# Kernel optimization log

Hardware: AMD Instinct MI355X
Metric: run time of the kernel (lower is better)

Reference implementation:

```python
import jax, jax.numpy as jnp
import numpy as np

B, DIM, H, W = 16, 96, 64, 64
HID = 2 * DIM          # ffn_expansion_factor = 2
BN_EPS = 1e-5
LN_EPS = 1e-6


def _gelu(x):
    return jax.nn.gelu(x, approximate=False)  # torch F.gelu default = exact erf


def _ln(x, g, b):
    m = jnp.mean(x, axis=-1, keepdims=True)
    v = jnp.mean((x - m) ** 2, axis=-1, keepdims=True)
    return (x - m) / jnp.sqrt(v + LN_EPS) * g + b


def _dwconv2d(x, w, b):
    # x: (B,C,H,W), w: (C,1,kh,kw) depthwise
    C = x.shape[1]
    kh, kw = w.shape[2], w.shape[3]
    y = jax.lax.conv_general_dilated(
        x, w, (1, 1), [(kh // 2, kh // 2), (kw // 2, kw // 2)],
        dimension_numbers=('NCHW', 'OIHW', 'NCHW'), feature_group_count=C)
    return y + b[None, :, None, None]


def _conv_along_c(z, w, b):
    # z: (N,1,C); w: (8,1,k) -> conv over spectral/channel axis (Conv3d with (1,1,k) kernel)
    k = w.shape[2]
    y = jax.lax.conv_general_dilated(z, w, (1,), [(k // 2, k // 2)],
                                     dimension_numbers=('NCH', 'OIH', 'NCH'))
    return y + b[None, :, None]


def _bn_branch(y, g, bb):
    # eval-mode BatchNorm3d with running_mean=0, running_var=1; y: (N,8,C)
    return _gelu(y * (g / jnp.sqrt(1.0 + BN_EPS))[None, :, None] + bb[None, :, None])


def _patch_embed(z, w3a, b3a, bn3a_g, bn3a_b, w3b, b3b, bn3b_g, bn3b_b,
                 w3c, b3c, bn3c_g, bn3c_b, w2, b2, bn2_g, bn2_b):
    # z: (b,h,w,c) NHWC; PatchEmbedLayerSpa
    b_, h_, w_, c_ = z.shape
    zf = z.reshape(-1, 1, c_)
    f1 = _bn_branch(_conv_along_c(zf, w3a, b3a), bn3a_g, bn3a_b)
    f2 = _bn_branch(_conv_along_c(zf, w3b, b3b), bn3b_g, bn3b_b)
    f3 = _bn_branch(_conv_along_c(zf, w3c, b3c), bn3c_g, bn3c_b)
    cat = jnp.concatenate([f1, f2, f3], axis=1).reshape(b_, h_, w_, 24, c_)
    # 1x1 Conv2d over flattened (c y) -> dim; einsum replaces rearrange + conv
    y = jnp.einsum('bhwoy,doy->bhwd', cat, w2) + b2
    y = _gelu(y * (bn2_g / jnp.sqrt(1.0 + BN_EPS)) + bn2_b)  # eval BatchNorm2d + GELU
    return y + z


def _ffn(t, pin_w, pin_b, dw_w, dw_b, pout_w, pout_b):
    # Restormer GDFN; t: (b, c, X, Y) NCHW
    u = jnp.einsum('bcxy,oc->boxy', t, pin_w) + pin_b[None, :, None, None]
    u = _dwconv2d(u, dw_w, dw_b)
    u1, u2 = jnp.split(u, 2, axis=1)
    g = _gelu(u1) * u2
    return jnp.einsum('bcxy,oc->boxy', g, pout_w) + pout_b[None, :, None, None]


def setup_inputs() -> dict:
    key = jax.random.key(0)
    ks = iter(jax.random.split(key, 48))
    nrm = lambda shape, s=0.02: jax.random.normal(next(ks), shape, jnp.float32) * s
    d = {}
    d['x'] = jax.random.normal(next(ks), (B, DIM, H, W), jnp.float32)
    d['pos_w'] = nrm((DIM, 1, 3, 3)); d['pos_b'] = jnp.zeros((DIM,), jnp.float32)
    for n in ('ln1', 'ln2', 'ln3'):
        d[n + '_g'] = jnp.ones((DIM,), jnp.float32)
        d[n + '_b'] = jnp.zeros((DIM,), jnp.float32)
    for n, k in (('a', 3), ('b', 5), ('c', 7)):
        d['w3' + n] = nrm((8, 1, k)); d['b3' + n] = jnp.zeros((8,), jnp.float32)
        d['bn3' + n + '_g'] = jnp.ones((8,), jnp.float32)
        d['bn3' + n + '_b'] = jnp.zeros((8,), jnp.float32)
    d['w2'] = nrm((DIM, 24, DIM)); d['b2'] = jnp.zeros((DIM,), jnp.float32)
    d['bn2_g'] = jnp.ones((DIM,), jnp.float32); d['bn2_b'] = jnp.zeros((DIM,), jnp.float32)
    d['pin_w'] = nrm((2 * HID, DIM)); d['pin_b'] = jnp.zeros((2 * HID,), jnp.float32)
    d['dw_w'] = nrm((2 * HID, 1, 3, 3)); d['dw_b'] = jnp.zeros((2 * HID,), jnp.float32)
    d['pout_w'] = nrm((DIM, HID)); d['pout_b'] = jnp.zeros((DIM,), jnp.float32)
    return d


def reference(x, pos_w, pos_b, ln1_g, ln1_b, ln2_g, ln2_b, ln3_g, ln3_b,
              w3a, b3a, bn3a_g, bn3a_b, w3b, b3b, bn3b_g, bn3b_b,
              w3c, b3c, bn3c_g, bn3c_b, w2, b2, bn2_g, bn2_b,
              pin_w, pin_b, dw_w, dw_b, pout_w, pout_b):
    # pos embed dwconv + residual (NCHW)
    x = x + _dwconv2d(x, pos_w, pos_b)
    y = jnp.transpose(x, (0, 2, 3, 1))  # NHWC
    # attn4(norm3(y)) returns its input (bug in source: `out = rearrange(x, ...)`)
    y = y + _ln(y, ln3_g, ln3_b)
    # attn(norm1(y)) returns PatchEmbedLayerSpa(norm1(y)) (same bug in MGEFE)
    y = y + _patch_embed(_ln(y, ln1_g, ln1_b), w3a, b3a, bn3a_g, bn3a_b,
                         w3b, b3b, bn3b_g, bn3b_b, w3c, b3c, bn3c_g, bn3c_b,
                         w2, b2, bn2_g, bn2_b)
    y = _ln(y, ln2_g, ln2_b)
    t = jnp.transpose(y, (0, 3, 2, 1))  # (b,c,w,h) per source permute(0,3,2,1)
    f = _ffn(t, pin_w, pin_b, dw_w, dw_b, pout_w, pout_b)
    f = jnp.transpose(f, (0, 2, 3, 1))  # (b,w,h,c)
    y = f + f
    return jnp.transpose(y, (0, 3, 1, 2))  # (b,c,w,h)
```

## Files before the change

### kernel.cpp

```cpp
#include <hip/hip_runtime.h>


using bf16x8 = __attribute__((ext_vector_type(8))) short;
using f32x4  = __attribute__((ext_vector_type(4))) float;
using f32x2  = __attribute__((ext_vector_type(2))) float;

struct P {
  const float *x, *pos_w, *pos_b;
  const float *ln1g, *ln1b, *ln2g, *ln2b, *ln3g, *ln3b;
  const float *w3a, *b3a, *bn3ag, *bn3ab;
  const float *w3b, *b3b, *bn3bg, *bn3bb;
  const float *w3c, *b3c, *bn3cg, *bn3cb;
  const float *w2, *b2, *bn2g, *bn2b;
  const float *pin_w, *pin_b, *dw_w, *dw_b, *pout_w, *pout_b;
  float *y1;
  unsigned short *u;
  unsigned short *w2f;
  unsigned short *pinf;
  unsigned short *poutf;
  float *dwt;
  float *out;
};

__device__ __forceinline__ unsigned short f2bf(float f) {
  unsigned int v = __float_as_uint(f);
  v += 0x7fffu + ((v >> 16) & 1u);
  return (unsigned short)(v >> 16);
}
__device__ __forceinline__ float bf2f(unsigned short s) {
  return __uint_as_float(((unsigned int)s) << 16);
}
__device__ __forceinline__ unsigned int cvtpk(f32x2 g) {
  unsigned int pk;
  asm("v_cvt_pk_bf16_f32 %0, %1, %2" : "=v"(pk) : "v"(g.x), "v"(g.y));
  return pk;
}

__device__ __forceinline__ f32x2 gelu2p(f32x2 x) {
  f32x2 u = x * 0.70710678118654752f;
  f32x2 s = __builtin_elementwise_min(u * u, f32x2{1.f, 1.f});
  f32x2 pq = __builtin_elementwise_fma(s, f32x2{1.1283585149e-1f, 1.1283585149e-1f},
                                       f32x2{-3.7612625824e-1f, -3.7612625824e-1f});
  pq = __builtin_elementwise_fma(pq, s, f32x2{1.1283791657f, 1.1283791657f});
  f32x2 xh = x * 0.5f;
  return __builtin_elementwise_fma(xh, u * pq, xh);
}

__device__ __forceinline__ void swz_decode(int bid, int& b, int& s) {
  int xcd = bid & 7, idx = bid >> 3;
  b = xcd * 2 + (idx >> 6);
  s = idx & 63;
}

__global__ __launch_bounds__(256) void k1p(P p) {
  __shared__ float t1[96 * 65];
  if (blockIdx.x >= 1024) {
    int id = (blockIdx.x - 1024) * 256 + threadIdx.x;
    if (id < 221184) {
      int j = id & 7, l = (id >> 3) & 63, r = id >> 9;
      int ks = r % 3; r /= 3; int nt = r % 6, o = r / 6;
      int d = nt * 16 + (l & 15), y = ks * 32 + (l >> 4) * 8 + j;
      p.w2f[id] = f2bf(p.w2[(d * 24 + o) * 96 + y]);
    } else if (id < 258048) {
      int id2 = id - 221184;
      int j = id2 & 7, l = (id2 >> 3) & 63, r = id2 >> 9;
      int ks = r % 3, nt = r / 3;
      int o = nt * 16 + (l & 15), k = ks * 32 + (l >> 4) * 8 + j;
      p.pinf[id2] = f2bf(p.pin_w[o * 96 + k]);
    } else if (id < 276480) {
      int id3 = id - 258048;
      int j = id3 & 7, l = (id3 >> 3) & 63, r = id3 >> 9;
      int ks = r % 6, mt = r / 6;
      int d = mt * 16 + (l & 15), cc = ks * 32 + (l >> 4) * 8 + j;
      p.poutf[id3] = f2bf(p.pout_w[d * 192 + cc]);
    } else if (id < 279936) {
      int id4 = id - 276480;
      int tap = id4 / 384, c = id4 - tap * 384;
      p.dwt[id4] = p.dw_w[c * 9 + tap];
    }
    return;
  }

  int b, h; swz_decode(blockIdx.x, b, h);
  int bh = b * 64 + h;
  int t = threadIdx.x;
  const float* xb = p.x + (size_t)b * 96 * 4096;

  if (t < 192) {
    int c = t >> 1, w0 = (t & 1) * 32;
    const float* xc = xb + (size_t)c * 4096;
    float win[3][34];
    #pragma unroll
    for (int r = 0; r < 3; ++r) {
      int hh = h - 1 + r;
      bool v = (hh >= 0 && hh < 64);
      const float* row = xc + hh * 64;
      #pragma unroll
      for (int i = 0; i < 8; ++i) {
        float4 q = v ? *(const float4*)(row + w0 + i * 4) : make_float4(0,0,0,0);
        win[r][1+i*4] = q.x; win[r][2+i*4] = q.y;
        win[r][3+i*4] = q.z; win[r][4+i*4] = q.w;
      }
      win[r][0]  = (v && w0 > 0)  ? row[w0 - 1]  : 0.f;
      win[r][33] = (v && w0 < 32) ? row[w0 + 32] : 0.f;
    }
    float wt[9];
    #pragma unroll
    for (int i = 0; i < 9; ++i) wt[i] = p.pos_w[c * 9 + i];
    float pb = p.pos_b[c];
    #pragma unroll
    for (int w = 0; w < 32; ++w) {
      float acc = pb;
      #pragma unroll
      for (int r = 0; r < 3; ++r)
        #pragma unroll
        for (int j = 0; j < 3; ++j)
          acc = fmaf(wt[r * 3 + j], win[r][w + j], acc);
      t1[c * 65 + w0 + w] = win[1][w + 1] + acc;
    }
  }
  __syncthreads();
  {
    int w = t >> 2, c0 = (t & 3) * 24;
    float vv[24];
    float s1 = 0.f, s2 = 0.f;
    #pragma unroll
    for (int i = 0; i < 24; ++i) {
      float q = t1[(c0 + i) * 65 + w];
      vv[i] = q; s1 += q; s2 += q * q;
    }
    s1 += __shfl_xor(s1, 1); s1 += __shfl_xor(s1, 2);
    s2 += __shfl_xor(s2, 1); s2 += __shfl_xor(s2, 2);
    float m = s1 * (1.f / 96.f);
    float r = rsqrtf(fmaf(-m, m, s2 * (1.f / 96.f)) + 1e-6f);
    #pragma unroll
    for (int i = 0; i < 24; ++i) {
      int c = c0 + i;
      vv[i] += fmaf((vv[i] - m) * r, p.ln3g[c], p.ln3b[c]);
    }
    float* dst = p.y1 + (size_t)bh * 6144 + w * 96 + c0;
    #pragma unroll
    for (int i = 0; i < 6; ++i)
      *(float4*)(dst + i * 4) = make_float4(vv[i*4], vv[i*4+1], vv[i*4+2], vv[i*4+3]);
  }
}

template <int KSZ>
__device__ __forceinline__ void k2_cat(const float* __restrict__ w3, float b3v,
    float bng, float bnb, float rs, unsigned short* buf,
    const float (&zw)[30], int px, int c0) {
  float sc = bng * rs;
  float wr[KSZ];
  #pragma unroll
  for (int k = 0; k < KSZ; ++k) wr[k] = w3[k] * sc;
  float bias0 = fmaf(b3v, sc, bnb);
  constexpr int OFF = 3 - KSZ / 2;
  unsigned int packed[12];
  #pragma unroll
  for (int e2 = 0; e2 < 12; ++e2) {
    f32x2 f = {bias0, bias0};
    #pragma unroll
    for (int k = 0; k < KSZ; ++k) {
      f32x2 zp = {zw[2 * e2 + OFF + k], zw[2 * e2 + 1 + OFF + k]};
      f = __builtin_elementwise_fma(f32x2{wr[k], wr[k]}, zp, f);
    }
    packed[e2] = cvtpk(gelu2p(f));
  }
  uint4* cw = (uint4*)(buf + px * 104 + c0);
  cw[0] = *(uint4*)&packed[0];
  cw[1] = *(uint4*)&packed[4];
  cw[2] = *(uint4*)&packed[8];
}

template <int KSZ_NEXT, bool LAST>
__device__ __forceinline__ void k2_step(
    const P& p, int o, const float* __restrict__ w3n, float b3n,
    float bngn, float bnbn, float rs,
    const unsigned short* cur, unsigned short* nxt, const float (&zw)[30],
    int px, int c0, int nt0, int ar0, int ar1, f32x4 (&acc)[2][3]) {
  int lane = (threadIdx.x & 63);
  const unsigned short* wf = p.w2f + (size_t)o * 9216 + lane * 8;
  bf16x8 Ba[3], Bb[3];
  #pragma unroll
  for (int n = 0; n < 3; ++n)
    Ba[n] = *(const bf16x8*)(wf + ((nt0 + n) * 3 + 0) * 512);

  if (!LAST)
    k2_cat<KSZ_NEXT>(w3n, b3n, bngn, bnbn, rs, nxt, zw, px, c0);

  #pragma unroll
  for (int n = 0; n < 3; ++n)
    Bb[n] = *(const bf16x8*)(wf + ((nt0 + n) * 3 + 1) * 512);
  {
    bf16x8 a0 = *(const bf16x8*)&cur[ar0];
    bf16x8 a1 = *(const bf16x8*)&cur[ar1];
    #pragma unroll
    for (int n = 0; n < 3; ++n) {
      acc[0][n] = __builtin_amdgcn_mfma_f32_16x16x32_bf16(a0, Ba[n], acc[0][n], 0, 0, 0);
      acc[1][n] = __builtin_amdgcn_mfma_f32_16x16x32_bf16(a1, Ba[n], acc[1][n], 0, 0, 0);
    }
  }
  #pragma unroll
  for (int n = 0; n < 3; ++n)
    Ba[n] = *(const bf16x8*)(wf + ((nt0 + n) * 3 + 2) * 512);
  {
    bf16x8 a0 = *(const bf16x8*)&cur[ar0 + 32];
    bf16x8 a1 = *(const bf16x8*)&cur[ar1 + 32];
    #pragma unroll
    for (int n = 0; n < 3; ++n) {
      acc[0][n] = __builtin_amdgcn_mfma_f32_16x16x32_bf16(a0, Bb[n], acc[0][n], 0, 0, 0);
      acc[1][n] = __builtin_amdgcn_mfma_f32_16x16x32_bf16(a1, Bb[n], acc[1][n], 0, 0, 0);
    }
  }
  {
    bf16x8 a0 = *(const bf16x8*)&cur[ar0 + 64];
    bf16x8 a1 = *(const bf16x8*)&cur[ar1 + 64];
    #pragma unroll
    for (int n = 0; n < 3; ++n) {
      acc[0][n] = __builtin_amdgcn_mfma_f32_16x16x32_bf16(a0, Ba[n], acc[0][n], 0, 0, 0);
      acc[1][n] = __builtin_amdgcn_mfma_f32_16x16x32_bf16(a1, Ba[n], acc[1][n], 0, 0, 0);
    }
  }
  __syncthreads();
}

__global__ __launch_bounds__(256) void k2(P p) {
  __shared__ __align__(16) char smraw[26624];
  unsigned short* cat0 = (unsigned short*)smraw;
  unsigned short* cat1 = (unsigned short*)(smraw + 13312);

  int b, h; swz_decode(blockIdx.x, b, h);
  int bh = b * 64 + h;
  int t = threadIdx.x, lane = t & 63, wv = t >> 6;
  const float* yrow = p.y1 + (size_t)bh * 6144;
  int px = t >> 2, sub = t & 3, c0 = sub * 24;

  float zw[30];
  {
    float v[24];
    const float* src = yrow + px * 96 + c0;
    float s1 = 0.f, s2 = 0.f;
    #pragma unroll
    for (int i = 0; i < 6; ++i) {
      float4 q = *(const float4*)(src + i * 4);
      v[i*4] = q.x; v[i*4+1] = q.y; v[i*4+2] = q.z; v[i*4+3] = q.w;
    }
    #pragma unroll
    for (int i = 0; i < 24; ++i) { s1 += v[i]; s2 += v[i] * v[i]; }
    s1 += __shfl_xor(s1, 1); s1 += __shfl_xor(s1, 2);
    s2 += __shfl_xor(s2, 1); s2 += __shfl_xor(s2, 2);
    float m = s1 * (1.f / 96.f);
    float r = rsqrtf(fmaf(-m, m, s2 * (1.f / 96.f)) + 1e-6f);
    #pragma unroll
    for (int i = 0; i < 24; ++i) {
      int c = c0 + i;
      zw[3 + i] = fmaf((v[i] - m) * r, p.ln1g[c], p.ln1b[c]);
    }
  }
  {
    float a0 = __shfl(zw[24], lane - 1), a1 = __shfl(zw[25], lane - 1),
          a2 = __shfl(zw[26], lane - 1);
    float b0 = __shfl(zw[3], lane + 1), b1 = __shfl(zw[4], lane + 1),
          b2 = __shfl(zw[5], lane + 1);
    bool lo = (sub > 0), hi = (sub < 3);
    zw[0] = lo ? a0 : 0.f; zw[1] = lo ? a1 : 0.f; zw[2] = lo ? a2 : 0.f;
    zw[27] = hi ? b0 : 0.f; zw[28] = hi ? b1 : 0.f; zw[29] = hi ? b2 : 0.f;
  }

  const float rs = rsqrtf(1.f + 1e-5f);
  const int m0 = (wv >> 1) * 32, nt0 = (wv & 1) * 3;
  const int lm = lane & 15, lq = lane >> 4;
  const int ar0 = (m0 + lm) * 104 + lq * 8, ar1 = ar0 + 16 * 104;
  f32x4 acc[2][3];
  #pragma unroll
  for (int m = 0; m < 2; ++m)
    #pragma unroll
    for (int n = 0; n < 3; ++n) acc[m][n] = (f32x4){0.f, 0.f, 0.f, 0.f};

  k2_cat<3>(p.w3a, p.b3a[0], p.bn3ag[0], p.bn3ab[0], rs, cat0, zw, px, c0);
  __syncthreads();

  for (int o = 0; o < 7; ++o)
    k2_step<3, false>(p, o, p.w3a + (o + 1) * 3, p.b3a[o + 1],
                      p.bn3ag[o + 1], p.bn3ab[o + 1], rs,
                      (o & 1) ? cat1 : cat0, (o & 1) ? cat0 : cat1,
                      zw, px, c0, nt0, ar0, ar1, acc);
  k2_step<5, false>(p, 7, p.w3b, p.b3b[0], p.bn3bg[0], p.bn3bb[0], rs,
                    cat1, cat0, zw, px, c0, nt0, ar0, ar1, acc);
  for (int o = 8; o < 15; ++o)
    k2_step<5, false>(p, o, p.w3b + (o - 7) * 5, p.b3b[o - 7],
                      p.bn3bg[o - 7], p.bn3bb[o - 7], rs,
                      (o & 1) ? cat1 : cat0, (o & 1) ? cat0 : cat1,
                      zw, px, c0, nt0, ar0, ar1, acc);
  k2_step<7, false>(p, 15, p.w3c, p.b3c[0], p.bn3cg[0], p.bn3cb[0], rs,
                    cat1, cat0, zw, px, c0, nt0, ar0, ar1, acc);
  for (int o = 16; o < 23; ++o)
    k2_step<7, false>(p, o, p.w3c + (o - 15) * 7, p.b3c[o - 15],
                      p.bn3cg[o - 15], p.bn3cb[o - 15], rs,
                      (o & 1) ? cat1 : cat0, (o & 1) ? cat0 : cat1,
                      zw, px, c0, nt0, ar0, ar1, acc);
  k2_step<3, true>(p, 23, p.w3a, 0.f, 0.f, 0.f, rs,
                   cat1, cat0, zw, px, c0, nt0, ar0, ar1, acc);

  #pragma unroll
  for (int mi = 0; mi < 2; ++mi)
    #pragma unroll
    for (int n = 0; n < 3; ++n) {
      int d = (nt0 + n) * 16 + lm;
      float sc2 = p.bn2g[d] * rs, sh2 = p.bn2b[d], bias = p.b2[d];
      int pxb = m0 + mi * 16 + lq * 4;
      unsigned int pk01 = cvtpk(gelu2p(f32x2{fmaf(acc[mi][n][0] + bias, sc2, sh2),
                                             fmaf(acc[mi][n][1] + bias, sc2, sh2)}));
      unsigned int pk23 = cvtpk(gelu2p(f32x2{fmaf(acc[mi][n][2] + bias, sc2, sh2),
                                             fmaf(acc[mi][n][3] + bias, sc2, sh2)}));
      cat0[(pxb+0) * 104 + d] = (unsigned short)(pk01 & 0xffffu);
      cat0[(pxb+1) * 104 + d] = (unsigned short)(pk01 >> 16);
      cat0[(pxb+2) * 104 + d] = (unsigned short)(pk23 & 0xffffu);
      cat0[(pxb+3) * 104 + d] = (unsigned short)(pk23 >> 16);
    }
  __syncthreads();

  {
    const float* src = yrow + px * 96 + c0;
    const unsigned int* gsrc = (const unsigned int*)(cat0 + px * 104 + c0);
    float vv[24];
    float s1 = 0.f, s2 = 0.f;
    #pragma unroll
    for (int i2 = 0; i2 < 6; ++i2) {
      float4 q = *(const float4*)(src + i2 * 4);
      unsigned int w0 = gsrc[i2 * 2], w1 = gsrc[i2 * 2 + 1];
      float g0 = __uint_as_float(w0 << 16), g1 = __uint_as_float(w0 & 0xffff0000u);
      float g2 = __uint_as_float(w1 << 16), g3 = __uint_as_float(w1 & 0xffff0000u);
      float y0v = g0 + zw[3 + i2*4 + 0] + q.x;
      float y1v = g1 + zw[3 + i2*4 + 1] + q.y;
      float y2v = g2 + zw[3 + i2*4 + 2] + q.z;
      float y3v = g3 + zw[3 + i2*4 + 3] + q.w;
      vv[i2*4+0] = y0v; vv[i2*4+1] = y1v; vv[i2*4+2] = y2v; vv[i2*4+3] = y3v;
      s1 += y0v + y1v + y2v + y3v;
      s2 += y0v*y0v + y1v*y1v + y2v*y2v + y3v*y3v;
    }
    s1 += __shfl_xor(s1, 1); s1 += __shfl_xor(s1, 2);
    s2 += __shfl_xor(s2, 1); s2 += __shfl_xor(s2, 2);
    float m = s1 * (1.f / 96.f);
    float r = rsqrtf(fmaf(-m, m, s2 * (1.f / 96.f)) + 1e-6f);
    unsigned int* dst = (unsigned int*)(cat1 + px * 104 + c0);
    #pragma unroll
    for (int i = 0; i < 12; ++i) {
      int c = c0 + 2 * i;
      f32x2 y3p = {fmaf((vv[2*i]   - m) * r, p.ln2g[c],     p.ln2b[c]),
                   fmaf((vv[2*i+1] - m) * r, p.ln2g[c + 1], p.ln2b[c + 1])};
      dst[i] = cvtpk(y3p);
    }
  }
  __syncthreads();

  {
    const int mt = wv;
    bf16x8 A3[3];
    #pragma unroll
    for (int ks = 0; ks < 3; ++ks)
      A3[ks] = *(const bf16x8*)&cat1[(mt * 16 + lm) * 104 + ks * 32 + lq * 8];
    unsigned short* ubh = p.u + (size_t)b * 1572864 + h * 384;

    bf16x8 Bn[3];
    const unsigned short* pf0 = p.pinf + lane * 8;
    #pragma unroll
    for (int ks = 0; ks < 3; ++ks)
      Bn[ks] = *(const bf16x8*)(pf0 + ks * 512);
    for (int nt = 0; nt < 24; ++nt) {
      bf16x8 Bf[3] = {Bn[0], Bn[1], Bn[2]};
      if (nt < 23) {
        const unsigned short* pf = p.pinf + ((nt + 1) * 3) * 512 + lane * 8;
        #pragma unroll
        for (int ks = 0; ks < 3; ++ks)
          Bn[ks] = *(const bf16x8*)(pf + ks * 512);
      }
      f32x4 a4 = (f32x4){0.f, 0.f, 0.f, 0.f};
      #pragma unroll
      for (int ks = 0; ks < 3; ++ks)
        a4 = __builtin_amdgcn_mfma_f32_16x16x32_bf16(A3[ks], Bf[ks], a4, 0, 0, 0);
      int c = nt * 16 + lm;
      float pbv = p.pin_b[c];
      #pragma unroll
      for (int r = 0; r < 4; ++r) {
        int w = mt * 16 + lq * 4 + r;
        ubh[(size_t)w * 24576 + c] = f2bf(a4[r] + pbv);
      }
    }
  }
}

__global__ __launch_bounds__(256) void k4(P p) {
  __shared__ __align__(16) char sm4[40960];
  float*          dwl = (float*)sm4;
  float*          dbl = (float*)(sm4 + 13824);
  unsigned short* gl  = (unsigned short*)(sm4 + 15360);

  int b, w; swz_decode(blockIdx.x, b, w);
  int t = threadIdx.x, lane = t & 63, wv = t >> 6;
  const unsigned short* ub = p.u + (size_t)b * 1572864;

  for (int id = t; id < 3456; id += 256) dwl[id] = p.dwt[id];
  for (int id = t; id < 384; id += 256) dbl[id] = p.dw_b[id];
  __syncthreads();

  if (t < 192) {
    int g = t / 24, cb = t - g * 24;
    int c0 = cb * 8, hb = g * 8;
    float4 b1a = *(const float4*)&dbl[c0],       b1b = *(const float4*)&dbl[c0 + 4];
    float4 b2a = *(const float4*)&dbl[192 + c0], b2b = *(const float4*)&dbl[196 + c0];
    const bf16x8 zv = {0,0,0,0,0,0,0,0};
    for (int kk = 0; kk < 4; ++kk) {
      int h0 = hb + kk * 2;
      float v1[2][8], v2[2][8];
      #pragma unroll
      for (int hr = 0; hr < 2; ++hr) {
        v1[hr][0]=b1a.x; v1[hr][1]=b1a.y; v1[hr][2]=b1a.z; v1[hr][3]=b1a.w;
        v1[hr][4]=b1b.x; v1[hr][5]=b1b.y; v1[hr][6]=b1b.z; v1[hr][7]=b1b.w;
        v2[hr][0]=b2a.x; v2[hr][1]=b2a.y; v2[hr][2]=b2a.z; v2[hr][3]=b2a.w;
        v2[hr][4]=b2b.x; v2[hr][5]=b2b.y; v2[hr][6]=b2b.z; v2[hr][7]=b2b.w;
      }
      #pragma unroll
      for (int dw_ = -1; dw_ <= 1; ++dw_) {
        int ww = w + dw_;
        if (ww < 0 || ww > 63) continue;
        bf16x8 r1[4], r2[4];
        #pragma unroll
        for (int rr = 0; rr < 4; ++rr) {
          int hh = h0 - 1 + rr;
          bool ok = (hh >= 0 && hh <= 63);
          const unsigned short* up = ub + ((size_t)ww * 64 + hh) * 384 + c0;
          r1[rr] = ok ? *(const bf16x8*)up : zv;
          r2[rr] = ok ? *(const bf16x8*)(up + 192) : zv;
        }
        #pragma unroll
        for (int dh = -1; dh <= 1; ++dh) {
          int tap = (dw_ + 1) * 3 + (dh + 1);
          float4 w1a = *(const float4*)&dwl[tap * 384 + c0];
          float4 w1b = *(const float4*)&dwl[tap * 384 + c0 + 4];
          float4 w2a = *(const float4*)&dwl[tap * 384 + 192 + c0];
          float4 w2b = *(const float4*)&dwl[tap * 384 + 196 + c0];
          float wt1[8] = {w1a.x,w1a.y,w1a.z,w1a.w,w1b.x,w1b.y,w1b.z,w1b.w};
          float wt2[8] = {w2a.x,w2a.y,w2a.z,w2a.w,w2b.x,w2b.y,w2b.z,w2b.w};
          #pragma unroll
          for (int hr = 0; hr < 2; ++hr) {
            int rr = hr + dh + 1;
            #pragma unroll
            for (int j = 0; j < 8; ++j) {
              v1[hr][j] = fmaf(wt1[j], bf2f((unsigned short)r1[rr][j]), v1[hr][j]);
              v2[hr][j] = fmaf(wt2[j], bf2f((unsigned short)r2[rr][j]), v2[hr][j]);
            }
          }
        }
      }
      #pragma unroll
      for (int hr = 0; hr < 2; ++hr) {
        unsigned int pk4[4];
        #pragma unroll
        for (int j2 = 0; j2 < 4; ++j2) {
          f32x2 a = {v1[hr][2*j2], v1[hr][2*j2+1]};
          f32x2 bv = {v2[hr][2*j2], v2[hr][2*j2+1]};
          pk4[j2] = cvtpk(gelu2p(a) * bv);
        }
        uint2* dst = (uint2*)(gl + (h0 + hr) * 200 + c0);
        dst[0] = make_uint2(pk4[0], pk4[1]);
        dst[1] = make_uint2(pk4[2], pk4[3]);
      }
    }
  }
  __syncthreads();

  const int lm = lane & 15, lq = lane >> 4;
  const int mt0 = (wv >> 1) * 3, nt0 = (wv & 1) * 2;
  bf16x8 Af[3][6];
  const unsigned short* pof = p.poutf + lane * 8;
  #pragma unroll
  for (int mi = 0; mi < 3; ++mi)
    #pragma unroll
    for (int ks = 0; ks < 6; ++ks)
      Af[mi][ks] = *(const bf16x8*)(pof + ((mt0 + mi) * 6 + ks) * 512);
  f32x4 acc[3][2];
  #pragma unroll
  for (int mi = 0; mi < 3; ++mi)
    #pragma unroll
    for (int n = 0; n < 2; ++n) acc[mi][n] = (f32x4){0.f, 0.f, 0.f, 0.f};
  #pragma unroll
  for (int ks = 0; ks < 6; ++ks) {
    bf16x8 Bg[2];
    #pragma unroll
    for (int n = 0; n < 2; ++n)
      Bg[n] = *(const bf16x8*)&gl[((nt0 + n) * 16 + lm) * 200 + ks * 32 + lq * 8];
    #pragma unroll
    for (int mi = 0; mi < 3; ++mi)
      #pragma unroll
      for (int n = 0; n < 2; ++n)
        acc[mi][n] = __builtin_amdgcn_mfma_f32_16x16x32_bf16(Af[mi][ks], Bg[n], acc[mi][n], 0, 0, 0);
  }
  float* ob = p.out + (size_t)b * 393216 + (size_t)w * 64;
  #pragma unroll
  for (int mi = 0; mi < 3; ++mi)
    #pragma unroll
    for (int r = 0; r < 4; ++r) {
      int d = (mt0 + mi) * 16 + lq * 4 + r;
      float pb = p.pout_b[d];
      #pragma unroll
      for (int n = 0; n < 2; ++n) {
        int hcol = (nt0 + n) * 16 + lm;
        ob[(size_t)d * 4096 + hcol] = 2.f * (acc[mi][n][r] + pb);
      }
    }
}

extern "C" void kernel_launch(void* const* d_in, const int* in_sizes, int n_in,
                              void* d_out, int out_size, void* d_ws, size_t ws_size,
                              hipStream_t stream) {
  (void)in_sizes; (void)n_in; (void)out_size; (void)ws_size;
  P p;
  p.x     = (const float*)d_in[0];
  p.pos_w = (const float*)d_in[1];  p.pos_b = (const float*)d_in[2];
  p.ln1g  = (const float*)d_in[3];  p.ln1b  = (const float*)d_in[4];
  p.ln2g  = (const float*)d_in[5];  p.ln2b  = (const float*)d_in[6];
  p.ln3g  = (const float*)d_in[7];  p.ln3b  = (const float*)d_in[8];
  p.w3a   = (const float*)d_in[9];  p.b3a   = (const float*)d_in[10];
  p.bn3ag = (const float*)d_in[11]; p.bn3ab = (const float*)d_in[12];
  p.w3b   = (const float*)d_in[13]; p.b3b   = (const float*)d_in[14];
  p.bn3bg = (const float*)d_in[15]; p.bn3bb = (const float*)d_in[16];
  p.w3c   = (const float*)d_in[17]; p.b3c   = (const float*)d_in[18];
  p.bn3cg = (const float*)d_in[19]; p.bn3cb = (const float*)d_in[20];
  p.w2    = (const float*)d_in[21]; p.b2    = (const float*)d_in[22];
  p.bn2g  = (const float*)d_in[23]; p.bn2b  = (const float*)d_in[24];
  p.pin_w = (const float*)d_in[25]; p.pin_b = (const float*)d_in[26];
  p.dw_w  = (const float*)d_in[27]; p.dw_b  = (const float*)d_in[28];
  p.pout_w= (const float*)d_in[29]; p.pout_b= (const float*)d_in[30];

  char* ws = (char*)d_ws;
  p.y1    = (float*)ws;
  p.u     = (unsigned short*)(ws + 25165824);
  p.poutf = (unsigned short*)(ws + 75497472);
  p.dwt   = (float*)(ws + 75534336);
  p.w2f   = (unsigned short*)d_out;
  p.pinf  = (unsigned short*)((char*)d_out + 442368);
  p.out   = (float*)d_out;

  k1p<<<dim3(2118), dim3(256), 0, stream>>>(p);
  k2 <<<dim3(1024), dim3(256), 0, stream>>>(p);
  k4 <<<dim3(1024), dim3(256), 0, stream>>>(p);
}
```

Before: 176.8 us.

## Stage w2 weights into LDS asynchronously, transpose pin GEMM stores, shrink k4 block

New measurement: 168.1 us. -4.9%, faster.

```diff
diff --git a/kernel.cpp b/kernel.cpp
--- a/kernel.cpp
+++ b/kernel.cpp
@@ -34,6 +34,11 @@
   unsigned int pk;
   asm("v_cvt_pk_bf16_f32 %0, %1, %2" : "=v"(pk) : "v"(g.x), "v"(g.y));
   return pk;
+}
+__device__ __forceinline__ void gld16(const unsigned short* g, unsigned short* l) {
+  __builtin_amdgcn_global_load_lds(
+      (const __attribute__((address_space(1))) unsigned int*)g,
+      (__attribute__((address_space(3))) unsigned int*)l, 16, 0, 0);
 }
 
 __device__ __forceinline__ f32x2 gelu2p(f32x2 x) {
@@ -145,6 +150,17 @@
   }
 }
 
+__device__ __forceinline__ void stage_w2(const P& p, int o,
+                                         unsigned short* wdst, int wv, int lane) {
+  const unsigned short* src = p.w2f + (size_t)o * 9216 + lane * 8;
+  #pragma unroll
+  for (int ch = 0; ch < 5; ++ch) {
+    int c = wv + ch * 4;
+    if (c < 18)
+      gld16(src + c * 512, wdst + c * 512);
+  }
+}
+
 template <int KSZ>
 __device__ __forceinline__ void k2_cat(const float* __restrict__ w3, float b3v,
     float bng, float bnb, float rs, unsigned short* buf,
@@ -176,18 +192,22 @@
 __device__ __forceinline__ void k2_step(
     const P& p, int o, const float* __restrict__ w3n, float b3n,
     float bngn, float bnbn, float rs,
-    const unsigned short* cur, unsigned short* nxt, const float (&zw)[30],
+    const unsigned short* cur, unsigned short* nxt,
+    const unsigned short* wcur, unsigned short* wnxt, const float (&zw)[30],
     int px, int c0, int nt0, int ar0, int ar1, f32x4 (&acc)[2][3]) {
-  int lane = (threadIdx.x & 63);
-  const unsigned short* wf = p.w2f + (size_t)o * 9216 + lane * 8;
+  int lane = (threadIdx.x & 63), wv = (threadIdx.x >> 6);
+
+  if (!LAST)
+    stage_w2(p, o + 1, wnxt, wv, lane);
+
+  if (!LAST)
+    k2_cat<KSZ_NEXT>(w3n, b3n, bngn, bnbn, rs, nxt, zw, px, c0);
+
+  const unsigned short* wf = wcur + lane * 8;
   bf16x8 Ba[3], Bb[3];
   #pragma unroll
   for (int n = 0; n < 3; ++n)
     Ba[n] = *(const bf16x8*)(wf + ((nt0 + n) * 3 + 0) * 512);
-
-  if (!LAST)
-    k2_cat<KSZ_NEXT>(w3n, b3n, bngn, bnbn, rs, nxt, zw, px, c0);
-
   #pragma unroll
   for (int n = 0; n < 3; ++n)
     Bb[n] = *(const bf16x8*)(wf + ((nt0 + n) * 3 + 1) * 512);
@@ -225,9 +245,11 @@
 }
 
 __global__ __launch_bounds__(256) void k2(P p) {
-  __shared__ __align__(16) char smraw[26624];
+  __shared__ __align__(16) char smraw[63488];
   unsigned short* cat0 = (unsigned short*)smraw;
   unsigned short* cat1 = (unsigned short*)(smraw + 13312);
+  unsigned short* wb0  = (unsigned short*)(smraw + 26624);
+  unsigned short* wb1  = (unsigned short*)(smraw + 45056);
 
   int b, h; swz_decode(blockIdx.x, b, h);
   int bh = b * 64 + h;
@@ -277,6 +299,7 @@
     #pragma unroll
     for (int n = 0; n < 3; ++n) acc[m][n] = (f32x4){0.f, 0.f, 0.f, 0.f};
 
+  stage_w2(p, 0, wb0, wv, lane);
   k2_cat<3>(p.w3a, p.b3a[0], p.bn3ag[0], p.bn3ab[0], rs, cat0, zw, px, c0);
   __syncthreads();
 
@@ -284,23 +307,26 @@
     k2_step<3, false>(p, o, p.w3a + (o + 1) * 3, p.b3a[o + 1],
                       p.bn3ag[o + 1], p.bn3ab[o + 1], rs,
                       (o & 1) ? cat1 : cat0, (o & 1) ? cat0 : cat1,
+                      (o & 1) ? wb1 : wb0, (o & 1) ? wb0 : wb1,
                       zw, px, c0, nt0, ar0, ar1, acc);
   k2_step<5, false>(p, 7, p.w3b, p.b3b[0], p.bn3bg[0], p.bn3bb[0], rs,
-                    cat1, cat0, zw, px, c0, nt0, ar0, ar1, acc);
+                    cat1, cat0, wb1, wb0, zw, px, c0, nt0, ar0, ar1, acc);
   for (int o = 8; o < 15; ++o)
     k2_step<5, false>(p, o, p.w3b + (o - 7) * 5, p.b3b[o - 7],
                       p.bn3bg[o - 7], p.bn3bb[o - 7], rs,
                       (o & 1) ? cat1 : cat0, (o & 1) ? cat0 : cat1,
+                      (o & 1) ? wb1 : wb0, (o & 1) ? wb0 : wb1,
                       zw, px, c0, nt0, ar0, ar1, acc);
   k2_step<7, false>(p, 15, p.w3c, p.b3c[0], p.bn3cg[0], p.bn3cb[0], rs,
-                    cat1, cat0, zw, px, c0, nt0, ar0, ar1, acc);
+                    cat1, cat0, wb1, wb0, zw, px, c0, nt0, ar0, ar1, acc);
   for (int o = 16; o < 23; ++o)
     k2_step<7, false>(p, o, p.w3c + (o - 15) * 7, p.b3c[o - 15],
                       p.bn3cg[o - 15], p.bn3cb[o - 15], rs,
                       (o & 1) ? cat1 : cat0, (o & 1) ? cat0 : cat1,
+                      (o & 1) ? wb1 : wb0, (o & 1) ? wb0 : wb1,
                       zw, px, c0, nt0, ar0, ar1, acc);
   k2_step<3, true>(p, 23, p.w3a, 0.f, 0.f, 0.f, rs,
-                   cat1, cat0, zw, px, c0, nt0, ar0, ar1, acc);
+                   cat1, cat0, wb1, wb0, zw, px, c0, nt0, ar0, ar1, acc);
 
   #pragma unroll
   for (int mi = 0; mi < 2; ++mi)
@@ -356,41 +382,40 @@
 
   {
     const int mt = wv;
-    bf16x8 A3[3];
+    bf16x8 B3[3];
     #pragma unroll
     for (int ks = 0; ks < 3; ++ks)
-      A3[ks] = *(const bf16x8*)&cat1[(mt * 16 + lm) * 104 + ks * 32 + lq * 8];
+      B3[ks] = *(const bf16x8*)&cat1[(mt * 16 + lm) * 104 + ks * 32 + lq * 8];
     unsigned short* ubh = p.u + (size_t)b * 1572864 + h * 384;
-
-    bf16x8 Bn[3];
+    const int w = mt * 16 + lm;
+    unsigned short* urow = ubh + (size_t)w * 24576 + lq * 4;
+
+    bf16x8 An[3];
     const unsigned short* pf0 = p.pinf + lane * 8;
     #pragma unroll
     for (int ks = 0; ks < 3; ++ks)
-      Bn[ks] = *(const bf16x8*)(pf0 + ks * 512);
+      An[ks] = *(const bf16x8*)(pf0 + ks * 512);
     for (int nt = 0; nt < 24; ++nt) {
-      bf16x8 Bf[3] = {Bn[0], Bn[1], Bn[2]};
+      bf16x8 Af[3] = {An[0], An[1], An[2]};
       if (nt < 23) {
         const unsigned short* pf = p.pinf + ((nt + 1) * 3) * 512 + lane * 8;
         #pragma unroll
         for (int ks = 0; ks < 3; ++ks)
-          Bn[ks] = *(const bf16x8*)(pf + ks * 512);
+          An[ks] = *(const bf16x8*)(pf + ks * 512);
       }
       f32x4 a4 = (f32x4){0.f, 0.f, 0.f, 0.f};
       #pragma unroll
       for (int ks = 0; ks < 3; ++ks)
-        a4 = __builtin_amdgcn_mfma_f32_16x16x32_bf16(A3[ks], Bf[ks], a4, 0, 0, 0);
-      int c = nt * 16 + lm;
-      float pbv = p.pin_b[c];
-      #pragma unroll
-      for (int r = 0; r < 4; ++r) {
-        int w = mt * 16 + lq * 4 + r;
-        ubh[(size_t)w * 24576 + c] = f2bf(a4[r] + pbv);
-      }
-    }
-  }
-}
-
-__global__ __launch_bounds__(256) void k4(P p) {
+        a4 = __builtin_amdgcn_mfma_f32_16x16x32_bf16(Af[ks], B3[ks], a4, 0, 0, 0);
+      float4 pbq = *(const float4*)(p.pin_b + nt * 16 + lq * 4);
+      unsigned int lo = cvtpk(f32x2{a4[0] + pbq.x, a4[1] + pbq.y});
+      unsigned int hi = cvtpk(f32x2{a4[2] + pbq.z, a4[3] + pbq.w});
+      *(uint2*)(urow + nt * 16) = make_uint2(lo, hi);
+    }
+  }
+}
+
+__global__ __launch_bounds__(192) void k4(P p) {
   __shared__ __align__(16) char sm4[40960];
   float*          dwl = (float*)sm4;
   float*          dbl = (float*)(sm4 + 13824);
@@ -400,11 +425,11 @@
   int t = threadIdx.x, lane = t & 63, wv = t >> 6;
   const unsigned short* ub = p.u + (size_t)b * 1572864;
 
-  for (int id = t; id < 3456; id += 256) dwl[id] = p.dwt[id];
-  for (int id = t; id < 384; id += 256) dbl[id] = p.dw_b[id];
-  __syncthreads();
-
-  if (t < 192) {
+  for (int id = t; id < 3456; id += 192) dwl[id] = p.dwt[id];
+  for (int id = t; id < 384; id += 192) dbl[id] = p.dw_b[id];
+  __syncthreads();
+
+  {
     int g = t / 24, cb = t - g * 24;
     int c0 = cb * 8, hb = g * 8;
     float4 b1a = *(const float4*)&dbl[c0],       b1b = *(const float4*)&dbl[c0 + 4];
@@ -471,41 +496,41 @@
   __syncthreads();
 
   const int lm = lane & 15, lq = lane >> 4;
-  const int mt0 = (wv >> 1) * 3, nt0 = (wv & 1) * 2;
-  bf16x8 Af[3][6];
+  const int mtb = wv * 2;
+  bf16x8 Af[2][6];
   const unsigned short* pof = p.poutf + lane * 8;
   #pragma unroll
-  for (int mi = 0; mi < 3; ++mi)
+  for (int mi = 0; mi < 2; ++mi)
     #pragma unroll
     for (int ks = 0; ks < 6; ++ks)
-      Af[mi][ks] = *(const bf16x8*)(pof + ((mt0 + mi) * 6 + ks) * 512);
-  f32x4 acc[3][2];
-  #pragma unroll
-  for (int mi = 0; mi < 3; ++mi)
-    #pragma unroll
-    for (int n = 0; n < 2; ++n) acc[mi][n] = (f32x4){0.f, 0.f, 0.f, 0.f};
+      Af[mi][ks] = *(const bf16x8*)(pof + ((mtb + mi) * 6 + ks) * 512);
+  f32x4 acc[2][4];
+  #pragma unroll
+  for (int mi = 0; mi < 2; ++mi)
+    #pragma unroll
+    for (int n = 0; n < 4; ++n) acc[mi][n] = (f32x4){0.f, 0.f, 0.f, 0.f};
   #pragma unroll
   for (int ks = 0; ks < 6; ++ks) {
-    bf16x8 Bg[2];
-    #pragma unroll
-    for (int n = 0; n < 2; ++n)
-      Bg[n] = *(const bf16x8*)&gl[((nt0 + n) * 16 + lm) * 200 + ks * 32 + lq * 8];
-    #pragma unroll
-    for (int mi = 0; mi < 3; ++mi)
-      #pragma unroll
-      for (int n = 0; n < 2; ++n)
+    bf16x8 Bg[4];
+    #pragma unroll
+    for (int n = 0; n < 4; ++n)
+      Bg[n] = *(const bf16x8*)&gl[(n * 16 + lm) * 200 + ks * 32 + lq * 8];
+    #pragma unroll
+    for (int mi = 0; mi < 2; ++mi)
+      #pragma unroll
+      for (int n = 0; n < 4; ++n)
         acc[mi][n] = __builtin_amdgcn_mfma_f32_16x16x32_bf16(Af[mi][ks], Bg[n], acc[mi][n], 0, 0, 0);
   }
   float* ob = p.out + (size_t)b * 393216 + (size_t)w * 64;
   #pragma unroll
-  for (int mi = 0; mi < 3; ++mi)
+  for (int mi = 0; mi < 2; ++mi)
     #pragma unroll
     for (int r = 0; r < 4; ++r) {
-      int d = (mt0 + mi) * 16 + lq * 4 + r;
+      int d = (mtb + mi) * 16 + lq * 4 + r;
       float pb = p.pout_b[d];
       #pragma unroll
-      for (int n = 0; n < 2; ++n) {
-        int hcol = (nt0 + n) * 16 + lm;
+      for (int n = 0; n < 4; ++n) {
+        int hcol = n * 16 + lm;
         ob[(size_t)d * 4096 + hcol] = 2.f * (acc[mi][n][r] + pb);
       }
     }
@@ -544,5 +569,5 @@
 
   k1p<<<dim3(2118), dim3(256), 0, stream>>>(p);
   k2 <<<dim3(1024), dim3(256), 0, stream>>>(p);
-  k4 <<<dim3(1024), dim3(256), 0, stream>>>(p);
-}
+  k4 <<<dim3(1024), dim3(192), 0, stream>>>(p);
+}
```
